# Kernel optimization log

Measured on AMD Instinct MI355X. Metric: run time of the kernel, lower is better.

Reference implementation:

```python
import jax, jax.numpy as jnp
import numpy as np

L, D, H, DH, DI, V, S, B = 12, 768, 12, 64, 3072, 32000, 512, 2
LN_EPS = 1e-3  # keras LayerNormalization default epsilon

def _gelu(x):
    return x * 0.5 * (1.0 + jnp.tanh(np.sqrt(2.0 / np.pi).astype(np.float32) * (x + 0.044715 * x ** 3)))

def _layer_norm(x, g, b):
    mu = jnp.mean(x, axis=-1, keepdims=True)
    var = jnp.mean((x - mu) ** 2, axis=-1, keepdims=True)
    return (x - mu) * jax.lax.rsqrt(var + LN_EPS) * g + b

def _rel_shift(x, klen):
    # x: [qlen, rlen, b, n] -> shifted [qlen, klen, b, n]
    q, r, b, n = x.shape
    x = x.reshape(r, q, b, n)[1:].reshape(q, r - 1, b, n)
    return x[:, :klen]

def _pos_emb():
    # relative positions klen..-qlen+1 (attn_type='bi', mems=None -> klen=qlen=S)
    pos_seq = jnp.arange(S, -S, -1.0, dtype=jnp.float32)                      # [2S]
    inv_freq = 1.0 / (10000.0 ** (jnp.arange(0, D, 2, dtype=jnp.float32) / D))
    sinusoid = pos_seq[:, None] * inv_freq[None, :]
    pe = jnp.concatenate([jnp.sin(sinusoid), jnp.cos(sinusoid)], axis=-1)     # [2S, D]
    return jnp.broadcast_to(pe[:, None, :], (2 * S, B, D))                    # [2S, B, D]

def setup_inputs() -> dict:
    key = jax.random.key(0)
    ks = jax.random.split(key, 12)
    rn = lambda k, sh: 0.02 * jax.random.normal(k, sh, dtype=jnp.float32)
    return {
        "inp_k": jax.random.randint(ks[0], (S, B), 0, V),
        "seg_ids": jax.random.randint(ks[1], (S, B), 0, 2),
        "input_mask": jax.random.randint(ks[2], (S, B), 0, 2),
        "lookup_table": rn(ks[3], (V, D)),
        "Wq": rn(ks[4], (L, D, H, DH)),
        "Wk": rn(ks[5], (L, D, H, DH)),
        "Wv": rn(ks[6], (L, D, H, DH)),
        "Wr": rn(ks[7], (L, D, H, DH)),
        "Wo": rn(ks[8], (L, D, H, DH)),
        "r_w_bias": rn(ks[9], (L, H, DH)),
        "r_r_bias": rn(ks[10], (L, H, DH)),
        "r_s_bias": rn(ks[11], (L, H, DH)),
        "seg_embed": rn(jax.random.fold_in(key, 100), (L, 2, H, DH)),
        "ln_attn_g": jnp.ones((L, D), jnp.float32),
        "ln_attn_b": jnp.zeros((L, D), jnp.float32),
        "ln_ff_g": jnp.ones((L, D), jnp.float32),
        "ln_ff_b": jnp.zeros((L, D), jnp.float32),
        "ff_w1": rn(jax.random.fold_in(key, 101), (L, D, DI)),
        "ff_b1": jnp.zeros((L, DI), jnp.float32),
        "ff_w2": rn(jax.random.fold_in(key, 102), (L, DI, D)),
        "ff_b2": jnp.zeros((L, D), jnp.float32),
    }

def reference(inp_k, seg_ids, input_mask, lookup_table, Wq, Wk, Wv, Wr, Wo,
              r_w_bias, r_r_bias, r_s_bias, seg_embed,
              ln_attn_g, ln_attn_b, ln_ff_g, ln_ff_b,
              ff_w1, ff_b1, ff_w2, ff_b2):
    h = lookup_table[inp_k]                                                   # [S,B,D]
    r = _pos_emb()                                                            # [2S,B,D]
    # segment "same/different" one-hot matrix [q,k,b,2]
    seg_mat = jax.nn.one_hot((seg_ids[:, None, :] != seg_ids[None, :, :]).astype(jnp.int32), 2, dtype=jnp.float32)
    attn_mask = input_mask.astype(jnp.float32)[None, :, :, None]              # [1,S,B,1] broadcast over q,heads
    scale = DH ** -0.5
    for l in range(L):
        q = jnp.einsum('ibh,hnd->ibnd', h, Wq[l])
        k = jnp.einsum('ibh,hnd->ibnd', h, Wk[l])
        v = jnp.einsum('ibh,hnd->ibnd', h, Wv[l])
        kr = jnp.einsum('ibh,hnd->ibnd', r, Wr[l])                            # [2S,B,n,d]
        ac = jnp.einsum('ibnd,jbnd->ijbn', q + r_w_bias[l], k)
        bd = _rel_shift(jnp.einsum('ibnd,jbnd->ijbn', q + r_r_bias[l], kr), S)
        ef = jnp.einsum('ibnd,snd->ibns', q + r_s_bias[l], seg_embed[l])
        ef = jnp.einsum('ijbs,ibns->ijbn', seg_mat, ef)
        score = (ac + bd + ef) * scale - 1e30 * attn_mask
        prob = jax.nn.softmax(score, axis=1)                                  # softmax over key axis j
        vec = jnp.einsum('ijbn,jbnd->ibnd', prob, v)
        h = _layer_norm(jnp.einsum('ibnd,hnd->ibh', vec, Wo[l]) + h, ln_attn_g[l], ln_attn_b[l])
        ff = _gelu(jnp.einsum('ibd,df->ibf', h, ff_w1[l]) + ff_b1[l])
        ff = jnp.einsum('ibf,fd->ibd', ff, ff_w2[l]) + ff_b2[l]
        h = _layer_norm(ff + h, ln_ff_g[l], ln_ff_b[l])
    return h
```

## Files before the change

### kernel.cpp

```cpp
#include <hip/hip_runtime.h>
#include <hip/hip_bf16.h>
#include <math.h>

#define S 512
#define B 2
#define D 768
#define H 12
#define DH 64
#define DI 3072
#define NL 12
#define NTOK (S * B)

typedef __attribute__((ext_vector_type(8))) short short8v;
typedef __attribute__((ext_vector_type(4))) float f32x4;

__device__ __forceinline__ unsigned short f2b(float f) {
  union { float f; unsigned int u; } v; v.f = f;
  unsigned int r = v.u + 0x7fffu + ((v.u >> 16) & 1u);
  return (unsigned short)(r >> 16);
}
__device__ __forceinline__ float b2f(unsigned short u) {
  union { unsigned int u; float f; } v; v.u = ((unsigned int)u) << 16;
  return v.f;
}

__device__ __forceinline__ float gelu_f(float x) {
  const float c = 0.7978845608028654f;
  float t = tanhf(c * (x + 0.044715f * x * x * x));
  return x * 0.5f * (1.0f + t);
}

__global__ __launch_bounds__(256) void embed_kernel(const int* __restrict__ inp_k,
                                                    const float* __restrict__ lut,
                                                    float* __restrict__ h,
                                                    unsigned short* __restrict__ h_bf) {
  int t = blockIdx.x;
  int id = inp_k[t];
  for (int j = threadIdx.x; j < D; j += 256) {
    float v = lut[(size_t)id * D + j];
    h[t * D + j] = v;
    h_bf[t * D + j] = f2b(v);
  }
}

__global__ __launch_bounds__(384) void posemb_kernel(unsigned short* __restrict__ r2b) {
  int j = blockIdx.x;
  int d = threadIdx.x;
  float pos = (float)(S - j);
  float inv_freq = expf(-logf(10000.0f) * (2.0f * (float)d / (float)D));
  float x = pos * inv_freq;
  r2b[j * D + d]       = f2b(sinf(x));
  r2b[j * D + 384 + d] = f2b(cosf(x));
}

__device__ __forceinline__ void transpose_swz(const float* __restrict__ src,
                                              unsigned short* __restrict__ dst,
                                              int K, int N, int tile, int n_base,
                                              unsigned short* __restrict__ Ls ) {
  int ntk = K >> 6;
  int tk = tile % ntk, tn = tile / ntk;
  int k0 = tk << 6, n0 = tn << 6;
  int tid = threadIdx.x;
  int kk = tid >> 4, c4 = (tid & 15) * 4;
#pragma unroll
  for (int r = 0; r < 4; ++r) {
    int k = kk + r * 16;
    float4 a = *(const float4*)&src[(size_t)(k0 + k) * N + n0 + c4];
    Ls[(c4 + 0) * 72 + k] = f2b(a.x);
    Ls[(c4 + 1) * 72 + k] = f2b(a.y);
    Ls[(c4 + 2) * 72 + k] = f2b(a.z);
    Ls[(c4 + 3) * 72 + k] = f2b(a.w);
  }
  __syncthreads();
  int nl = tid >> 2, kc0 = (tid & 3) << 4;
  int ng = n_base + n0;
  size_t tilebase = ((size_t)(ng >> 7) * ntk + tk) * 8192;
  int row = (ng & 64) + nl;
  int key = (row & 7) << 3;
  short8v v0 = *(short8v*)&Ls[nl * 72 + kc0];
  short8v v1 = *(short8v*)&Ls[nl * 72 + kc0 + 8];
  *(short8v*)&dst[tilebase + row * 64 + (kc0 ^ key)] = v0;
  *(short8v*)&dst[tilebase + row * 64 + ((kc0 + 8) ^ key)] = v1;
}

__global__ __launch_bounds__(256) void prep_all(const float* __restrict__ Wq,
                                                const float* __restrict__ Wk,
                                                const float* __restrict__ Wv,
                                                const float* __restrict__ Wr,
                                                const float* __restrict__ Wo,
                                                const float* __restrict__ W1,
                                                const float* __restrict__ W2,
                                                unsigned short* __restrict__ wqkv_t,
                                                unsigned short* __restrict__ wr_t,
                                                unsigned short* __restrict__ wo_t,
                                                unsigned short* __restrict__ w1_t,
                                                unsigned short* __restrict__ w2_t) {
  __shared__ __align__(16) unsigned short Ls[64 * 72];
  const size_t DD = (size_t)D * D;
  const size_t DDI = (size_t)D * DI;
  int tb = blockIdx.x;
  int l = tb / 1872, t2 = tb % 1872;
  int tid = threadIdx.x;
  if (t2 < 432) {
    int which = t2 / 144, tile = t2 % 144;
    const float* src = (which == 0 ? Wq : (which == 1 ? Wk : Wv)) + l * DD;
    transpose_swz(src, wqkv_t + l * 3 * DD, D, D, tile, which * D, Ls);
  } else if (t2 < 576) {
    transpose_swz(Wr + l * DD, wr_t + l * DD, D, D, t2 - 432, 0, Ls);
  } else if (t2 < 1152) {
    transpose_swz(W1 + l * DDI, w1_t + l * DDI, D, DI, t2 - 576, 0, Ls);
  } else if (t2 < 1728) {
    transpose_swz(W2 + l * DDI, w2_t + l * DDI, DI, D, t2 - 1152, 0, Ls);
  } else {
    int c = t2 - 1728;
    int tkk = c % 12, tnn = c / 12;
    int k0 = tkk << 6, n0 = tnn << 6;
    int nl = tid >> 2, kc0 = (tid & 3) << 4;
    const float* srcp = Wo + l * DD + (size_t)(n0 + nl) * D + k0 + kc0;
    float4 a0 = *(const float4*)&srcp[0];
    float4 a1 = *(const float4*)&srcp[4];
    float4 a2 = *(const float4*)&srcp[8];
    float4 a3 = *(const float4*)&srcp[12];
    short8v v0, v1;
    v0[0] = (short)f2b(a0.x); v0[1] = (short)f2b(a0.y); v0[2] = (short)f2b(a0.z); v0[3] = (short)f2b(a0.w);
    v0[4] = (short)f2b(a1.x); v0[5] = (short)f2b(a1.y); v0[6] = (short)f2b(a1.z); v0[7] = (short)f2b(a1.w);
    v1[0] = (short)f2b(a2.x); v1[1] = (short)f2b(a2.y); v1[2] = (short)f2b(a2.z); v1[3] = (short)f2b(a2.w);
    v1[4] = (short)f2b(a3.x); v1[5] = (short)f2b(a3.y); v1[6] = (short)f2b(a3.z); v1[7] = (short)f2b(a3.w);
    unsigned short* dst = wo_t + l * DD;
    size_t tilebase = ((size_t)(n0 >> 7) * 12 + tkk) * 8192;
    int row = (n0 & 64) + nl;
    int key = (row & 7) << 3;
    *(short8v*)&dst[tilebase + row * 64 + (kc0 ^ key)] = v0;
    *(short8v*)&dst[tilebase + row * 64 + ((kc0 + 8) ^ key)] = v1;
  }
}

template <int ACT, int OUTBF>
__device__ __forceinline__ void gemm_tile(const unsigned short* __restrict__ A,
                                          const unsigned short* __restrict__ Wt,
                                          const float* __restrict__ bias,
                                          float* __restrict__ Cf,
                                          unsigned short* __restrict__ Cb,
                                          int N, int K, int bm, int bn,
                                          int kbeg, int kend) {
  __shared__ __align__(16) unsigned short As[64 * 64];
  __shared__ __align__(16) unsigned short Bs[128 * 64];
  const int tid = threadIdx.x, lane = tid & 63, w = tid >> 6;
  const int l8 = lane >> 3, lm8 = lane & 7;
  const int aColByte = ((lm8 ^ l8) << 4);
  const int KT = K >> 6;
  const size_t wtn = (size_t)(bn >> 7) * KT;

  f32x4 acc[4][2];
#pragma unroll
  for (int mi = 0; mi < 4; ++mi)
#pragma unroll
    for (int ni = 0; ni < 2; ++ni)
      acc[mi][ni] = (f32x4){0.f, 0.f, 0.f, 0.f};

  for (int kt = kbeg; kt < kend; kt += 64) {
    __syncthreads();
#pragma unroll
    for (int c = 0; c < 2; ++c) {
      int row = c * 32 + w * 8 + l8;
      const char* src = (const char*)&A[(size_t)(bm + row) * K + kt] + aColByte;
      __builtin_amdgcn_global_load_lds(
          (const __attribute__((address_space(1))) void*)src,
          (__attribute__((address_space(3))) void*)((char*)As + c * 4096 + w * 1024),
          16, 0, 0);
    }
    const char* wt = (const char*)&Wt[(wtn + (kt >> 6)) * 8192];
#pragma unroll
    for (int c = 0; c < 4; ++c) {
      __builtin_amdgcn_global_load_lds(
          (const __attribute__((address_space(1))) void*)(wt + c * 4096 + w * 1024 + lane * 16),
          (__attribute__((address_space(3))) void*)((char*)Bs + c * 4096 + w * 1024),
          16, 0, 0);
    }
    __syncthreads();
#pragma unroll
    for (int ks = 0; ks < 2; ++ks) {
      const int kus = ks * 32 + (lane >> 4) * 8;
      short8v af[4], bf[2];
#pragma unroll
      for (int mi = 0; mi < 4; ++mi) {
        int row = mi * 16 + (lane & 15);
        af[mi] = *(const short8v*)&As[row * 64 + (kus ^ ((row & 7) << 3))];
      }
#pragma unroll
      for (int ni = 0; ni < 2; ++ni) {
        int row = w * 32 + ni * 16 + (lane & 15);
        bf[ni] = *(const short8v*)&Bs[row * 64 + (kus ^ ((row & 7) << 3))];
      }
#pragma unroll
      for (int mi = 0; mi < 4; ++mi)
#pragma unroll
        for (int ni = 0; ni < 2; ++ni)
          acc[mi][ni] = __builtin_amdgcn_mfma_f32_16x16x32_bf16(af[mi], bf[ni], acc[mi][ni], 0, 0, 0);
    }
  }

  int r0 = (lane >> 4) * 4, cc = lane & 15;
#pragma unroll
  for (int mi = 0; mi < 4; ++mi) {
    int row = bm + mi * 16 + r0;
#pragma unroll
    for (int ni = 0; ni < 2; ++ni) {
      int col = bn + w * 32 + ni * 16 + cc;
      float bv = bias ? bias[col] : 0.0f;
#pragma unroll
      for (int r = 0; r < 4; ++r) {
        float v = acc[mi][ni][r] + bv;
        if (ACT == 1) v = gelu_f(v);
        if (OUTBF) Cb[(size_t)(row + r) * N + col] = f2b(v);
        else       Cf[(size_t)(row + r) * N + col] = v;
      }
    }
  }
}

__global__ __launch_bounds__(256) void gemm_qkvkr(const unsigned short* __restrict__ h_bf,
                                                  const unsigned short* __restrict__ wqkv,
                                                  const unsigned short* __restrict__ r2_bf,
                                                  const unsigned short* __restrict__ wr,
                                                  unsigned short* __restrict__ qkv_bf,
                                                  unsigned short* __restrict__ kr_bf) {
  int bx = blockIdx.x;
  const unsigned short *A, *W;
  unsigned short* C;
  int N, bm, bn;
  if (bx < 288) {
    A = h_bf; W = wqkv; C = qkv_bf; N = 2304;
    bm = (bx / 18) * 64; bn = (bx % 18) * 128;
  } else {
    int b2 = bx - 288;
    A = r2_bf; W = wr; C = kr_bf; N = 768;
    bm = (b2 / 6) * 64; bn = (b2 % 6) * 128;
  }
  gemm_tile<0, 1>(A, W, nullptr, nullptr, C, N, 768, bm, bn, 0, 768);
}

template <int ACT>
__global__ __launch_bounds__(256) void gemm_bias(const unsigned short* __restrict__ A,
                                                 const unsigned short* __restrict__ W,
                                                 const float* __restrict__ bias,
                                                 unsigned short* __restrict__ C,
                                                 int N, int K, int ncb) {
  int bx = blockIdx.x;
  gemm_tile<ACT, 1>(A, W, bias, nullptr, C, N, K, (bx / ncb) * 64, (bx % ncb) * 128, 0, K);
}

__global__ __launch_bounds__(256) void gemm_splitk(const unsigned short* __restrict__ A,
                                                   const unsigned short* __restrict__ W,
                                                   float* __restrict__ part,
                                                   int N, int K, int kch) {
  int kz = blockIdx.z;
  float* Cf = part + (size_t)kz * NTOK * N;
  gemm_tile<0, 0>(A, W, nullptr, Cf, nullptr, N, K,
                  blockIdx.y * 64, blockIdx.x * 128, kz * kch, (kz + 1) * kch);
}

__global__ __launch_bounds__(256) void attn_kernel(const unsigned short* __restrict__ qkv,
                                                   const unsigned short* __restrict__ krb,
                                                   const int* __restrict__ seg_ids,
                                                   const int* __restrict__ input_mask,
                                                   const float* __restrict__ rwb,
                                                   const float* __restrict__ rrb,
                                                   const float* __restrict__ rsb,
                                                   const float* __restrict__ segemb,
                                                   float* __restrict__ scg,
                                                   unsigned short* __restrict__ vec_bf) {
  __shared__ __align__(16) char smem[64512];
  unsigned short* qw_s = (unsigned short*)(smem + 0);
  unsigned short* qr_s = (unsigned short*)(smem + 9216);
  unsigned short* k_s  = (unsigned short*)(smem + 18432);
  unsigned short* kr_s = (unsigned short*)(smem + 27648);
  unsigned short* bd_s = (unsigned short*)(smem + 46080);
  float* efs    = (float*)(smem + 63488);
  float* rinv_s = (float*)(smem + 64000);
  int*   segrow = (int*)(smem + 64256);
  unsigned short* pb_s = (unsigned short*)(smem + 0);
  unsigned short* vt_s = (unsigned short*)(smem + 9216);

  const int it = blockIdx.x * 64, b = blockIdx.y, n = blockIdx.z;
  const int tid = threadIdx.x, lane = tid & 63, w = tid >> 6;
  float* sc = scg + (size_t)((blockIdx.z * 2 + blockIdx.y) * 8 + blockIdx.x) * (64 * 512);

  {
    int il = tid >> 2, d16 = (tid & 3) * 16;
    int t = (it + il) * B + b;
    short8v q0 = *(const short8v*)&qkv[(size_t)t * 2304 + n * 64 + d16];
    short8v q1 = *(const short8v*)&qkv[(size_t)t * 2304 + n * 64 + d16 + 8];
    short8v ow0, ow1, or0, or1;
#pragma unroll
    for (int e = 0; e < 8; ++e) {
      float f0 = b2f((unsigned short)q0[e]);
      float f1 = b2f((unsigned short)q1[e]);
      ow0[e] = (short)f2b(f0 + rwb[n * 64 + d16 + e]);
      ow1[e] = (short)f2b(f1 + rwb[n * 64 + d16 + 8 + e]);
      or0[e] = (short)f2b(f0 + rrb[n * 64 + d16 + e]);
      or1[e] = (short)f2b(f1 + rrb[n * 64 + d16 + 8 + e]);
    }
    *(short8v*)&qw_s[il * 72 + d16] = ow0;
    *(short8v*)&qw_s[il * 72 + d16 + 8] = ow1;
    *(short8v*)&qr_s[il * 72 + d16] = or0;
    *(short8v*)&qr_s[il * 72 + d16 + 8] = or1;
  }
  if (tid < 128) {
    int il = tid >> 1, s = tid & 1;
    int t = (it + il) * B + b;
    float acc = 0.0f;
    for (int d = 0; d < 64; ++d)
      acc = fmaf(b2f(qkv[(size_t)t * 2304 + n * 64 + d]) + rsb[n * 64 + d],
                 segemb[(s * H + n) * 64 + d], acc);
    efs[s * 64 + il] = acc;
  }
  if (tid < 64) segrow[tid] = seg_ids[(it + tid) * B + b];

  for (int jt = 0; jt < 512; jt += 64) {
    __syncthreads();
    {
#pragma unroll
      for (int c = 0; c < 2; ++c) {
        int idx = tid + c * 256;
        int row = idx >> 3, k8 = (idx & 7) * 8;
        *(short8v*)&k_s[row * 72 + k8] =
            *(const short8v*)&qkv[(size_t)((jt + row) * B + b) * 2304 + 768 + n * 64 + k8];
      }
      int u0 = 448 - it + jt;
#pragma unroll
      for (int c = 0; c < 4; ++c) {
        int idx = tid + c * 256;
        int row = idx >> 3, k8 = (idx & 7) * 8;
        *(short8v*)&kr_s[row * 72 + k8] =
            *(const short8v*)&krb[(size_t)(u0 + row) * 768 + n * 64 + k8];
      }
    }
    __syncthreads();

    f32x4 aac[4], abd[4][2];
#pragma unroll
    for (int mi = 0; mi < 4; ++mi) {
      aac[mi] = (f32x4){0.f, 0.f, 0.f, 0.f};
      abd[mi][0] = (f32x4){0.f, 0.f, 0.f, 0.f};
      abd[mi][1] = (f32x4){0.f, 0.f, 0.f, 0.f};
    }
#pragma unroll
    for (int ks = 0; ks < 2; ++ks) {
      int kb = ks * 32 + (lane >> 4) * 8;
      short8v aw[4], ar[4];
#pragma unroll
      for (int mi = 0; mi < 4; ++mi) {
        aw[mi] = *(const short8v*)&qw_s[(mi * 16 + (lane & 15)) * 72 + kb];
        ar[mi] = *(const short8v*)&qr_s[(mi * 16 + (lane & 15)) * 72 + kb];
      }
      short8v bk  = *(const short8v*)&k_s[(w * 16 + (lane & 15)) * 72 + kb];
      short8v br0 = *(const short8v*)&kr_s[(w * 32 + (lane & 15)) * 72 + kb];
      short8v br1 = *(const short8v*)&kr_s[(w * 32 + 16 + (lane & 15)) * 72 + kb];
#pragma unroll
      for (int mi = 0; mi < 4; ++mi) {
        aac[mi] = __builtin_amdgcn_mfma_f32_16x16x32_bf16(aw[mi], bk, aac[mi], 0, 0, 0);
        abd[mi][0] = __builtin_amdgcn_mfma_f32_16x16x32_bf16(ar[mi], br0, abd[mi][0], 0, 0, 0);
        abd[mi][1] = __builtin_amdgcn_mfma_f32_16x16x32_bf16(ar[mi], br1, abd[mi][1], 0, 0, 0);
      }
    }
#pragma unroll
    for (int mi = 0; mi < 4; ++mi)
#pragma unroll
      for (int ni = 0; ni < 2; ++ni)
#pragma unroll
        for (int r = 0; r < 4; ++r)
          bd_s[(mi * 16 + (lane >> 4) * 4 + r) * 136 + w * 32 + ni * 16 + (lane & 15)] =
              f2b(abd[mi][ni][r]);
    __syncthreads();

    {
      int jl = w * 16 + (lane & 15);
      int jg = jt + jl;
      float maskterm = -1e30f * (float)input_mask[jg * B + b];
      int segj = seg_ids[jg * B + b];
#pragma unroll
      for (int mi = 0; mi < 4; ++mi)
#pragma unroll
        for (int r = 0; r < 4; ++r) {
          int il = mi * 16 + (lane >> 4) * 4 + r;
          float bd = b2f(bd_s[il * 136 + 64 - il + jl]);
          float e = efs[(segrow[il] != segj ? 1 : 0) * 64 + il];
          sc[il * 512 + jg] = (aac[mi][r] + bd + e) * 0.125f + maskterm;
        }
    }
  }
  __syncthreads();

  int srow = tid >> 2;
  float mx = -3.4e38f;
  {
    int c0 = (tid & 3) * 128;
    for (int c = 0; c < 128; c += 4) {
      float4 vv = *(const float4*)&sc[srow * 512 + c0 + c];
      mx = fmaxf(mx, fmaxf(fmaxf(vv.x, vv.y), fmaxf(vv.z, vv.w)));
    }
    mx = fmaxf(mx, __shfl_xor(mx, 1, 4));
    mx = fmaxf(mx, __shfl_xor(mx, 2, 4));
  }

  f32x4 acc_v[4];
#pragma unroll
  for (int mi = 0; mi < 4; ++mi) acc_v[mi] = (f32x4){0.f, 0.f, 0.f, 0.f};
  float rsum = 0.0f;
  const int vkey = (w & 1) * 8;

  for (int jt = 0; jt < 512; jt += 64) {
    __syncthreads();
    {
      int c16 = (tid & 3) * 16;
#pragma unroll
      for (int half = 0; half < 2; ++half) {
        float4 fa = *(const float4*)&sc[srow * 512 + jt + c16 + half * 8];
        float4 fb = *(const float4*)&sc[srow * 512 + jt + c16 + half * 8 + 4];
        float e0 = __expf(fa.x - mx), e1 = __expf(fa.y - mx);
        float e2 = __expf(fa.z - mx), e3 = __expf(fa.w - mx);
        float e4 = __expf(fb.x - mx), e5 = __expf(fb.y - mx);
        float e6 = __expf(fb.z - mx), e7 = __expf(fb.w - mx);
        rsum += e0 + e1 + e2 + e3 + e4 + e5 + e6 + e7;
        short8v o;
        o[0] = (short)f2b(e0); o[1] = (short)f2b(e1);
        o[2] = (short)f2b(e2); o[3] = (short)f2b(e3);
        o[4] = (short)f2b(e4); o[5] = (short)f2b(e5);
        o[6] = (short)f2b(e6); o[7] = (short)f2b(e7);
        *(short8v*)&pb_s[srow * 72 + c16 + half * 8] = o;
      }
    }
    {
      int vj = tid >> 2, vd16 = (tid & 3) * 16;
      int key = (vd16 & 16) ? 8 : 0;
      short8v v0 = *(const short8v*)&qkv[(size_t)((jt + vj) * B + b) * 2304 + 1536 + n * 64 + vd16];
      short8v v1 = *(const short8v*)&qkv[(size_t)((jt + vj) * B + b) * 2304 + 1536 + n * 64 + vd16 + 8];
#pragma unroll
      for (int e = 0; e < 8; ++e) {
        vt_s[(vd16 + e) * 72 + (vj ^ key)] = (unsigned short)v0[e];
        vt_s[(vd16 + 8 + e) * 72 + (vj ^ key)] = (unsigned short)v1[e];
      }
    }
    __syncthreads();
#pragma unroll
    for (int ks = 0; ks < 2; ++ks) {
      int kb = ks * 32 + (lane >> 4) * 8;
      short8v bv = *(const short8v*)&vt_s[(w * 16 + (lane & 15)) * 72 + (kb ^ vkey)];
#pragma unroll
      for (int mi = 0; mi < 4; ++mi) {
        short8v ap = *(const short8v*)&pb_s[(mi * 16 + (lane & 15)) * 72 + kb];
        acc_v[mi] = __builtin_amdgcn_mfma_f32_16x16x32_bf16(ap, bv, acc_v[mi], 0, 0, 0);
      }
    }
  }
  rsum += __shfl_xor(rsum, 1, 4);
  rsum += __shfl_xor(rsum, 2, 4);
  if ((tid & 3) == 0) rinv_s[srow] = 1.0f / rsum;
  __syncthreads();

#pragma unroll
  for (int mi = 0; mi < 4; ++mi)
#pragma unroll
    for (int r = 0; r < 4; ++r) {
      int row = mi * 16 + (lane >> 4) * 4 + r;
      int d = w * 16 + (lane & 15);
      int t = (it + row) * B + b;
      vec_bf[(size_t)t * D + n * 64 + d] = f2b(acc_v[mi][r] * rinv_s[row]);
    }
}

template <int P, int HASBIAS>
__global__ __launch_bounds__(256) void add_ln_reduce(const float* __restrict__ part,
                                                     const float* __restrict__ bias,
                                                     float* __restrict__ h,
                                                     unsigned short* __restrict__ h_bf,
                                                     const float* __restrict__ g,
                                                     const float* __restrict__ bi) {
  int t = blockIdx.x;
  int tid = threadIdx.x;
  __shared__ float red[256];
  float v[3];
  float s = 0.0f;
#pragma unroll
  for (int j = 0; j < 3; ++j) {
    int c = tid + j * 256;
    float x = 0.0f;
#pragma unroll
    for (int p = 0; p < P; ++p)
      x += part[(size_t)p * NTOK * D + (size_t)t * D + c];
    if (HASBIAS) x += bias[c];
    v[j] = x + h[(size_t)t * D + c];
    s += v[j];
  }
  red[tid] = s;
  __syncthreads();
  for (int st = 128; st > 0; st >>= 1) {
    if (tid < st) red[tid] += red[tid + st];
    __syncthreads();
  }
  float mu = red[0] / (float)D;
  __syncthreads();
  float s2 = 0.0f;
#pragma unroll
  for (int j = 0; j < 3; ++j) {
    float dd = v[j] - mu;
    s2 += dd * dd;
  }
  red[tid] = s2;
  __syncthreads();
  for (int st = 128; st > 0; st >>= 1) {
    if (tid < st) red[tid] += red[tid + st];
    __syncthreads();
  }
  float var = red[0] / (float)D;
  float rstd = rsqrtf(var + 1e-3f);
  __syncthreads();
#pragma unroll
  for (int j = 0; j < 3; ++j) {
    int c = tid + j * 256;
    float o = (v[j] - mu) * rstd * g[c] + bi[c];
    h[(size_t)t * D + c] = o;
    h_bf[(size_t)t * D + c] = f2b(o);
  }
}

extern "C" void kernel_launch(void* const* d_in, const int* in_sizes, int n_in,
                              void* d_out, int out_size, void* d_ws, size_t ws_size,
                              hipStream_t stream) {
  const int*   inp_k      = (const int*)d_in[0];
  const int*   seg_ids    = (const int*)d_in[1];
  const int*   input_mask = (const int*)d_in[2];
  const float* lut        = (const float*)d_in[3];
  const float* Wq         = (const float*)d_in[4];
  const float* Wk         = (const float*)d_in[5];
  const float* Wv         = (const float*)d_in[6];
  const float* Wr         = (const float*)d_in[7];
  const float* Wo         = (const float*)d_in[8];
  const float* r_w_bias   = (const float*)d_in[9];
  const float* r_r_bias   = (const float*)d_in[10];
  const float* r_s_bias   = (const float*)d_in[11];
  const float* seg_embed  = (const float*)d_in[12];
  const float* ln_attn_g  = (const float*)d_in[13];
  const float* ln_attn_b  = (const float*)d_in[14];
  const float* ln_ff_g    = (const float*)d_in[15];
  const float* ln_ff_b    = (const float*)d_in[16];
  const float* ff_w1      = (const float*)d_in[17];
  const float* ff_b1      = (const float*)d_in[18];
  const float* ff_w2      = (const float*)d_in[19];
  const float* ff_b2      = (const float*)d_in[20];

  float* h = (float*)d_out;
  char* wp = (char*)d_ws;
  auto alloc = [&](size_t bytes) -> void* {
    void* p = (void*)wp;
    wp += (bytes + 255) & ~(size_t)255;
    return p;
  };
  const size_t TOKD = (size_t)NTOK * D;
  const size_t DD = (size_t)D * D;
  const size_t DDI = (size_t)D * DI;
  unsigned short* qkv_bf = (unsigned short*)alloc((size_t)NTOK * 2304 * 2);
  unsigned short* kr_bf  = (unsigned short*)alloc(TOKD * 2);
  unsigned short* h_bf   = (unsigned short*)alloc(TOKD * 2);
  unsigned short* r2_bf  = (unsigned short*)alloc(TOKD * 2);
  unsigned short* vec_bf = (unsigned short*)alloc(TOKD * 2);
  unsigned short* ff1_bf = (unsigned short*)alloc((size_t)NTOK * DI * 2);
  float* scg  = (float*)alloc((size_t)192 * 64 * 512 * 4);
  float* part = (float*)alloc((size_t)4 * TOKD * 4);
  unsigned short* wqkv_t = (unsigned short*)alloc((size_t)NL * 3 * DD * 2);
  unsigned short* wr_t   = (unsigned short*)alloc((size_t)NL * DD * 2);
  unsigned short* wo_t   = (unsigned short*)alloc((size_t)NL * DD * 2);
  unsigned short* w1_t   = (unsigned short*)alloc((size_t)NL * DDI * 2);
  unsigned short* w2_t   = (unsigned short*)alloc((size_t)NL * DDI * 2);

  prep_all<<<NL * 1872, 256, 0, stream>>>(Wq, Wk, Wv, Wr, Wo, ff_w1, ff_w2,
                                          wqkv_t, wr_t, wo_t, w1_t, w2_t);
  embed_kernel<<<NTOK, 256, 0, stream>>>(inp_k, lut, h, h_bf);
  posemb_kernel<<<2 * S, 384, 0, stream>>>(r2_bf);

  for (int l = 0; l < NL; ++l) {
    gemm_qkvkr<<<384, 256, 0, stream>>>(h_bf, wqkv_t + (size_t)l * 3 * DD,
                                        r2_bf, wr_t + (size_t)l * DD,
                                        qkv_bf, kr_bf);

    attn_kernel<<<dim3(8, B, H), 256, 0, stream>>>(
        qkv_bf, kr_bf, seg_ids, input_mask,
        r_w_bias + (size_t)l * D, r_r_bias + (size_t)l * D,
        r_s_bias + (size_t)l * D, seg_embed + (size_t)l * 2 * H * DH,
        scg, vec_bf);

    gemm_splitk<<<dim3(6, 16, 2), 256, 0, stream>>>(
        vec_bf, wo_t + (size_t)l * DD, part, D, D, 384);
    add_ln_reduce<2, 0><<<NTOK, 256, 0, stream>>>(
        part, nullptr, h, h_bf, ln_attn_g + (size_t)l * D, ln_attn_b + (size_t)l * D);

    gemm_bias<1><<<24 * 16, 256, 0, stream>>>(
        h_bf, w1_t + (size_t)l * DDI, ff_b1 + (size_t)l * DI, ff1_bf, DI, D, 24);

    gemm_splitk<<<dim3(6, 16, 4), 256, 0, stream>>>(
        ff1_bf, w2_t + (size_t)l * DDI, part, D, DI, 768);
    add_ln_reduce<4, 1><<<NTOK, 256, 0, stream>>>(
        part, ff_b2 + (size_t)l * D, h, h_bf, ln_ff_g + (size_t)l * D, ln_ff_b + (size_t)l * D);
  }
}
```

Before: 1.427 ms.

## Fuse attention into a single-pass online-softmax loop, dropping the global score buffer

```diff
diff --git a/kernel.cpp b/kernel.cpp
--- a/kernel.cpp
+++ b/kernel.cpp
@@ -28,6 +28,10 @@
   const float c = 0.7978845608028654f;
   float t = tanhf(c * (x + 0.044715f * x * x * x));
   return x * 0.5f * (1.0f + t);
+}
+
+__device__ __forceinline__ int vkey(int r) {
+  return (((r & 7) ^ ((r >> 3) & 7)) << 3);
 }
 
 __global__ __launch_bounds__(256) void embed_kernel(const int* __restrict__ inp_k,
@@ -268,23 +272,23 @@
                                                    const float* __restrict__ rrb,
                                                    const float* __restrict__ rsb,
                                                    const float* __restrict__ segemb,
-                                                   float* __restrict__ scg,
                                                    unsigned short* __restrict__ vec_bf) {
-  __shared__ __align__(16) char smem[64512];
+  __shared__ __align__(16) char smem[64768];
   unsigned short* qw_s = (unsigned short*)(smem + 0);
   unsigned short* qr_s = (unsigned short*)(smem + 9216);
   unsigned short* k_s  = (unsigned short*)(smem + 18432);
   unsigned short* kr_s = (unsigned short*)(smem + 27648);
   unsigned short* bd_s = (unsigned short*)(smem + 46080);
+  float* sc_s  = (float*)(smem + 18432);
+  unsigned short* pb_s = (unsigned short*)(smem + 46080);
+  unsigned short* vt_s = (unsigned short*)(smem + 54272);
   float* efs    = (float*)(smem + 63488);
-  float* rinv_s = (float*)(smem + 64000);
-  int*   segrow = (int*)(smem + 64256);
-  unsigned short* pb_s = (unsigned short*)(smem + 0);
-  unsigned short* vt_s = (unsigned short*)(smem + 9216);
+  float* frow_s = (float*)(smem + 64000);
+  float* rinv_s = (float*)(smem + 64256);
+  int*   segrow = (int*)(smem + 64512);
 
   const int it = blockIdx.x * 64, b = blockIdx.y, n = blockIdx.z;
   const int tid = threadIdx.x, lane = tid & 63, w = tid >> 6;
-  float* sc = scg + (size_t)((blockIdx.z * 2 + blockIdx.y) * 8 + blockIdx.x) * (64 * 512);
 
   {
     int il = tid >> 2, d16 = (tid & 3) * 16;
@@ -317,17 +321,161 @@
   }
   if (tid < 64) segrow[tid] = seg_ids[(it + tid) * B + b];
 
+  {
+#pragma unroll
+    for (int c = 0; c < 2; ++c) {
+      int idx = tid + c * 256;
+      int row = idx >> 3, k8 = (idx & 7) * 8;
+      *(short8v*)&k_s[row * 72 + k8] =
+          *(const short8v*)&qkv[(size_t)(row * B + b) * 2304 + 768 + n * 64 + k8];
+    }
+    int u0 = 448 - it;
+#pragma unroll
+    for (int c = 0; c < 4; ++c) {
+      int idx = tid + c * 256;
+      int row = idx >> 3, k8 = (idx & 7) * 8;
+      *(short8v*)&kr_s[row * 72 + k8] =
+          *(const short8v*)&krb[(size_t)(u0 + row) * 768 + n * 64 + k8];
+    }
+  }
+
+  f32x4 acc_v[4];
+#pragma unroll
+  for (int mi = 0; mi < 4; ++mi) acc_v[mi] = (f32x4){0.f, 0.f, 0.f, 0.f};
+  float m_run = -3.0e38f;
+  float rsq = 0.0f;
+  const int srow = tid >> 2, sc0 = (tid & 3) * 16;
+
+  __syncthreads();
+
   for (int jt = 0; jt < 512; jt += 64) {
-    __syncthreads();
+    const int vj = tid >> 2, vd16 = (tid & 3) * 16;
+    short8v vl0 = *(const short8v*)&qkv[(size_t)((jt + vj) * B + b) * 2304 + 1536 + n * 64 + vd16];
+    short8v vl1 = *(const short8v*)&qkv[(size_t)((jt + vj) * B + b) * 2304 + 1536 + n * 64 + vd16 + 8];
+
+    f32x4 aac[4], abd[4][2];
+#pragma unroll
+    for (int mi = 0; mi < 4; ++mi) {
+      aac[mi] = (f32x4){0.f, 0.f, 0.f, 0.f};
+      abd[mi][0] = (f32x4){0.f, 0.f, 0.f, 0.f};
+      abd[mi][1] = (f32x4){0.f, 0.f, 0.f, 0.f};
+    }
+#pragma unroll
+    for (int ks = 0; ks < 2; ++ks) {
+      int kb = ks * 32 + (lane >> 4) * 8;
+      short8v aw[4], ar[4];
+#pragma unroll
+      for (int mi = 0; mi < 4; ++mi) {
+        aw[mi] = *(const short8v*)&qw_s[(mi * 16 + (lane & 15)) * 72 + kb];
+        ar[mi] = *(const short8v*)&qr_s[(mi * 16 + (lane & 15)) * 72 + kb];
+      }
+      short8v bk  = *(const short8v*)&k_s[(w * 16 + (lane & 15)) * 72 + kb];
+      short8v br0 = *(const short8v*)&kr_s[(w * 32 + (lane & 15)) * 72 + kb];
+      short8v br1 = *(const short8v*)&kr_s[(w * 32 + 16 + (lane & 15)) * 72 + kb];
+#pragma unroll
+      for (int mi = 0; mi < 4; ++mi) {
+        aac[mi] = __builtin_amdgcn_mfma_f32_16x16x32_bf16(aw[mi], bk, aac[mi], 0, 0, 0);
+        abd[mi][0] = __builtin_amdgcn_mfma_f32_16x16x32_bf16(ar[mi], br0, abd[mi][0], 0, 0, 0);
+        abd[mi][1] = __builtin_amdgcn_mfma_f32_16x16x32_bf16(ar[mi], br1, abd[mi][1], 0, 0, 0);
+      }
+    }
+#pragma unroll
+    for (int mi = 0; mi < 4; ++mi)
+#pragma unroll
+      for (int ni = 0; ni < 2; ++ni)
+#pragma unroll
+        for (int r = 0; r < 4; ++r)
+          bd_s[(mi * 16 + (lane >> 4) * 4 + r) * 136 + w * 32 + ni * 16 + (lane & 15)] =
+              f2b(abd[mi][ni][r]);
+    __syncthreads();
+
     {
+      int jl = w * 16 + (lane & 15);
+      int jg = jt + jl;
+      float maskterm = -1e30f * (float)input_mask[jg * B + b];
+      int segj = seg_ids[jg * B + b];
+#pragma unroll
+      for (int mi = 0; mi < 4; ++mi)
+#pragma unroll
+        for (int r = 0; r < 4; ++r) {
+          int il = mi * 16 + (lane >> 4) * 4 + r;
+          float bd = b2f(bd_s[il * 136 + 64 - il + jl]);
+          float e = efs[(segrow[il] != segj ? 1 : 0) * 64 + il];
+          sc_s[il * 68 + jl] = (aac[mi][r] + bd + e) * 0.125f + maskterm;
+        }
+    }
+    __syncthreads();
+
+    {
+      float4 f0 = *(const float4*)&sc_s[srow * 68 + sc0];
+      float4 f1 = *(const float4*)&sc_s[srow * 68 + sc0 + 4];
+      float4 f2 = *(const float4*)&sc_s[srow * 68 + sc0 + 8];
+      float4 f3 = *(const float4*)&sc_s[srow * 68 + sc0 + 12];
+      float mx = fmaxf(fmaxf(fmaxf(f0.x, f0.y), fmaxf(f0.z, f0.w)),
+                       fmaxf(fmaxf(f1.x, f1.y), fmaxf(f1.z, f1.w)));
+      mx = fmaxf(mx, fmaxf(fmaxf(fmaxf(f2.x, f2.y), fmaxf(f2.z, f2.w)),
+                           fmaxf(fmaxf(f3.x, f3.y), fmaxf(f3.z, f3.w))));
+      mx = fmaxf(mx, __shfl_xor(mx, 1, 4));
+      mx = fmaxf(mx, __shfl_xor(mx, 2, 4));
+      float mnew = fmaxf(m_run, mx);
+      float fsc = __expf(m_run - mnew);
+      m_run = mnew;
+      float p0 = __expf(f0.x - mnew), p1 = __expf(f0.y - mnew);
+      float p2 = __expf(f0.z - mnew), p3 = __expf(f0.w - mnew);
+      float p4 = __expf(f1.x - mnew), p5 = __expf(f1.y - mnew);
+      float p6 = __expf(f1.z - mnew), p7 = __expf(f1.w - mnew);
+      float p8 = __expf(f2.x - mnew), p9 = __expf(f2.y - mnew);
+      float pa = __expf(f2.z - mnew), pb = __expf(f2.w - mnew);
+      float pc = __expf(f3.x - mnew), pd = __expf(f3.y - mnew);
+      float pe = __expf(f3.z - mnew), pf = __expf(f3.w - mnew);
+      rsq = rsq * fsc + ((p0 + p1 + p2 + p3) + (p4 + p5 + p6 + p7)) +
+                        ((p8 + p9 + pa + pb) + (pc + pd + pe + pf));
+      short8v o0, o1;
+      o0[0] = (short)f2b(p0); o0[1] = (short)f2b(p1); o0[2] = (short)f2b(p2); o0[3] = (short)f2b(p3);
+      o0[4] = (short)f2b(p4); o0[5] = (short)f2b(p5); o0[6] = (short)f2b(p6); o0[7] = (short)f2b(p7);
+      o1[0] = (short)f2b(p8); o1[1] = (short)f2b(p9); o1[2] = (short)f2b(pa); o1[3] = (short)f2b(pb);
+      o1[4] = (short)f2b(pc); o1[5] = (short)f2b(pd); o1[6] = (short)f2b(pe); o1[7] = (short)f2b(pf);
+      int key = vkey(srow);
+      *(short8v*)&pb_s[srow * 64 + (sc0 ^ key)] = o0;
+      *(short8v*)&pb_s[srow * 64 + ((sc0 + 8) ^ key)] = o1;
+      if ((tid & 3) == 0) frow_s[srow] = fsc;
+#pragma unroll
+      for (int e = 0; e < 8; ++e) {
+        int d0 = vd16 + e, d1 = vd16 + 8 + e;
+        vt_s[d0 * 64 + (vj ^ vkey(d0))] = (unsigned short)vl0[e];
+        vt_s[d1 * 64 + (vj ^ vkey(d1))] = (unsigned short)vl1[e];
+      }
+    }
+    __syncthreads();
+
+#pragma unroll
+    for (int mi = 0; mi < 4; ++mi) {
+#pragma unroll
+      for (int r = 0; r < 4; ++r)
+        acc_v[mi][r] *= frow_s[mi * 16 + (lane >> 4) * 4 + r];
+    }
+#pragma unroll
+    for (int ks = 0; ks < 2; ++ks) {
+      int kb = ks * 32 + (lane >> 4) * 8;
+      int vrow = w * 16 + (lane & 15);
+      short8v bv = *(const short8v*)&vt_s[vrow * 64 + (kb ^ vkey(vrow))];
+#pragma unroll
+      for (int mi = 0; mi < 4; ++mi) {
+        int prow = mi * 16 + (lane & 15);
+        short8v ap = *(const short8v*)&pb_s[prow * 64 + (kb ^ vkey(prow))];
+        acc_v[mi] = __builtin_amdgcn_mfma_f32_16x16x32_bf16(ap, bv, acc_v[mi], 0, 0, 0);
+      }
+    }
+    if (jt < 448) {
+      int jn = jt + 64;
 #pragma unroll
       for (int c = 0; c < 2; ++c) {
         int idx = tid + c * 256;
         int row = idx >> 3, k8 = (idx & 7) * 8;
         *(short8v*)&k_s[row * 72 + k8] =
-            *(const short8v*)&qkv[(size_t)((jt + row) * B + b) * 2304 + 768 + n * 64 + k8];
-      }
-      int u0 = 448 - it + jt;
+            *(const short8v*)&qkv[(size_t)((jn + row) * B + b) * 2304 + 768 + n * 64 + k8];
+      }
+      int u0 = 448 - it + jn;
 #pragma unroll
       for (int c = 0; c < 4; ++c) {
         int idx = tid + c * 256;
@@ -337,126 +485,14 @@
       }
     }
     __syncthreads();
-
-    f32x4 aac[4], abd[4][2];
-#pragma unroll
-    for (int mi = 0; mi < 4; ++mi) {
-      aac[mi] = (f32x4){0.f, 0.f, 0.f, 0.f};
-      abd[mi][0] = (f32x4){0.f, 0.f, 0.f, 0.f};
-      abd[mi][1] = (f32x4){0.f, 0.f, 0.f, 0.f};
-    }
-#pragma unroll
-    for (int ks = 0; ks < 2; ++ks) {
-      int kb = ks * 32 + (lane >> 4) * 8;
-      short8v aw[4], ar[4];
-#pragma unroll
-      for (int mi = 0; mi < 4; ++mi) {
-        aw[mi] = *(const short8v*)&qw_s[(mi * 16 + (lane & 15)) * 72 + kb];
-        ar[mi] = *(const short8v*)&qr_s[(mi * 16 + (lane & 15)) * 72 + kb];
-      }
-      short8v bk  = *(const short8v*)&k_s[(w * 16 + (lane & 15)) * 72 + kb];
-      short8v br0 = *(const short8v*)&kr_s[(w * 32 + (lane & 15)) * 72 + kb];
-      short8v br1 = *(const short8v*)&kr_s[(w * 32 + 16 + (lane & 15)) * 72 + kb];
-#pragma unroll
-      for (int mi = 0; mi < 4; ++mi) {
-        aac[mi] = __builtin_amdgcn_mfma_f32_16x16x32_bf16(aw[mi], bk, aac[mi], 0, 0, 0);
-        abd[mi][0] = __builtin_amdgcn_mfma_f32_16x16x32_bf16(ar[mi], br0, abd[mi][0], 0, 0, 0);
-        abd[mi][1] = __builtin_amdgcn_mfma_f32_16x16x32_bf16(ar[mi], br1, abd[mi][1], 0, 0, 0);
-      }
-    }
-#pragma unroll
-    for (int mi = 0; mi < 4; ++mi)
-#pragma unroll
-      for (int ni = 0; ni < 2; ++ni)
-#pragma unroll
-        for (int r = 0; r < 4; ++r)
-          bd_s[(mi * 16 + (lane >> 4) * 4 + r) * 136 + w * 32 + ni * 16 + (lane & 15)] =
-              f2b(abd[mi][ni][r]);
-    __syncthreads();
-
-    {
-      int jl = w * 16 + (lane & 15);
-      int jg = jt + jl;
-      float maskterm = -1e30f * (float)input_mask[jg * B + b];
-      int segj = seg_ids[jg * B + b];
-#pragma unroll
-      for (int mi = 0; mi < 4; ++mi)
-#pragma unroll
-        for (int r = 0; r < 4; ++r) {
-          int il = mi * 16 + (lane >> 4) * 4 + r;
-          float bd = b2f(bd_s[il * 136 + 64 - il + jl]);
-          float e = efs[(segrow[il] != segj ? 1 : 0) * 64 + il];
-          sc[il * 512 + jg] = (aac[mi][r] + bd + e) * 0.125f + maskterm;
-        }
-    }
-  }
-  __syncthreads();
-
-  int srow = tid >> 2;
-  float mx = -3.4e38f;
+  }
+
   {
-    int c0 = (tid & 3) * 128;
-    for (int c = 0; c < 128; c += 4) {
-      float4 vv = *(const float4*)&sc[srow * 512 + c0 + c];
-      mx = fmaxf(mx, fmaxf(fmaxf(vv.x, vv.y), fmaxf(vv.z, vv.w)));
-    }
-    mx = fmaxf(mx, __shfl_xor(mx, 1, 4));
-    mx = fmaxf(mx, __shfl_xor(mx, 2, 4));
-  }
-
-  f32x4 acc_v[4];
-#pragma unroll
-  for (int mi = 0; mi < 4; ++mi) acc_v[mi] = (f32x4){0.f, 0.f, 0.f, 0.f};
-  float rsum = 0.0f;
-  const int vkey = (w & 1) * 8;
-
-  for (int jt = 0; jt < 512; jt += 64) {
-    __syncthreads();
-    {
-      int c16 = (tid & 3) * 16;
-#pragma unroll
-      for (int half = 0; half < 2; ++half) {
-        float4 fa = *(const float4*)&sc[srow * 512 + jt + c16 + half * 8];
-        float4 fb = *(const float4*)&sc[srow * 512 + jt + c16 + half * 8 + 4];
-        float e0 = __expf(fa.x - mx), e1 = __expf(fa.y - mx);
-        float e2 = __expf(fa.z - mx), e3 = __expf(fa.w - mx);
-        float e4 = __expf(fb.x - mx), e5 = __expf(fb.y - mx);
-        float e6 = __expf(fb.z - mx), e7 = __expf(fb.w - mx);
-        rsum += e0 + e1 + e2 + e3 + e4 + e5 + e6 + e7;
-        short8v o;
-        o[0] = (short)f2b(e0); o[1] = (short)f2b(e1);
-        o[2] = (short)f2b(e2); o[3] = (short)f2b(e3);
-        o[4] = (short)f2b(e4); o[5] = (short)f2b(e5);
-        o[6] = (short)f2b(e6); o[7] = (short)f2b(e7);
-        *(short8v*)&pb_s[srow * 72 + c16 + half * 8] = o;
-      }
-    }
-    {
-      int vj = tid >> 2, vd16 = (tid & 3) * 16;
-      int key = (vd16 & 16) ? 8 : 0;
-      short8v v0 = *(const short8v*)&qkv[(size_t)((jt + vj) * B + b) * 2304 + 1536 + n * 64 + vd16];
-      short8v v1 = *(const short8v*)&qkv[(size_t)((jt + vj) * B + b) * 2304 + 1536 + n * 64 + vd16 + 8];
-#pragma unroll
-      for (int e = 0; e < 8; ++e) {
-        vt_s[(vd16 + e) * 72 + (vj ^ key)] = (unsigned short)v0[e];
-        vt_s[(vd16 + 8 + e) * 72 + (vj ^ key)] = (unsigned short)v1[e];
-      }
-    }
-    __syncthreads();
-#pragma unroll
-    for (int ks = 0; ks < 2; ++ks) {
-      int kb = ks * 32 + (lane >> 4) * 8;
-      short8v bv = *(const short8v*)&vt_s[(w * 16 + (lane & 15)) * 72 + (kb ^ vkey)];
-#pragma unroll
-      for (int mi = 0; mi < 4; ++mi) {
-        short8v ap = *(const short8v*)&pb_s[(mi * 16 + (lane & 15)) * 72 + kb];
-        acc_v[mi] = __builtin_amdgcn_mfma_f32_16x16x32_bf16(ap, bv, acc_v[mi], 0, 0, 0);
-      }
-    }
-  }
-  rsum += __shfl_xor(rsum, 1, 4);
-  rsum += __shfl_xor(rsum, 2, 4);
-  if ((tid & 3) == 0) rinv_s[srow] = 1.0f / rsum;
+    float tot = rsq;
+    tot += __shfl_xor(tot, 1, 4);
+    tot += __shfl_xor(tot, 2, 4);
+    if ((tid & 3) == 0) rinv_s[srow] = 1.0f / tot;
+  }
   __syncthreads();
 
 #pragma unroll
@@ -566,7 +602,6 @@
   unsigned short* r2_bf  = (unsigned short*)alloc(TOKD * 2);
   unsigned short* vec_bf = (unsigned short*)alloc(TOKD * 2);
   unsigned short* ff1_bf = (unsigned short*)alloc((size_t)NTOK * DI * 2);
-  float* scg  = (float*)alloc((size_t)192 * 64 * 512 * 4);
   float* part = (float*)alloc((size_t)4 * TOKD * 4);
   unsigned short* wqkv_t = (unsigned short*)alloc((size_t)NL * 3 * DD * 2);
   unsigned short* wr_t   = (unsigned short*)alloc((size_t)NL * DD * 2);
@@ -588,7 +623,7 @@
         qkv_bf, kr_bf, seg_ids, input_mask,
         r_w_bias + (size_t)l * D, r_r_bias + (size_t)l * D,
         r_s_bias + (size_t)l * D, seg_embed + (size_t)l * 2 * H * DH,
-        scg, vec_bf);
+        vec_bf);
 
     gemm_splitk<<<dim3(6, 16, 2), 256, 0, stream>>>(
         vec_bf, wo_t + (size_t)l * DD, part, D, D, 384);
```

New measurement: 1.323 ms. 7.3% less time.
